# Performance work log

Measured on AMD Instinct MI355X. Metric: run time of the kernel, lower is better.

## Reference

```python
import jax, jax.numpy as jnp
import numpy as np

NUM_HEADS = 16
HIDDEN = 1024
HEAD_DIM = HIDDEN // NUM_HEADS


def setup_inputs() -> dict:
    key = jax.random.key(0)
    ks = jax.random.split(key, 9)
    B, S = 2, 2048
    s = 1.0 / np.sqrt(HIDDEN)
    return {
        "x": jax.random.normal(ks[0], (B, S, HIDDEN), dtype=jnp.float32),
        "Wq": jax.random.normal(ks[1], (HIDDEN, HIDDEN), dtype=jnp.float32) * s,
        "bq": jnp.zeros((HIDDEN,), dtype=jnp.float32),
        "Wk": jax.random.normal(ks[2], (HIDDEN, HIDDEN), dtype=jnp.float32) * s,
        "bk": jnp.zeros((HIDDEN,), dtype=jnp.float32),
        "Wv": jax.random.normal(ks[3], (HIDDEN, HIDDEN), dtype=jnp.float32) * s,
        "bv": jnp.zeros((HIDDEN,), dtype=jnp.float32),
        "Wo": jax.random.normal(ks[4], (HIDDEN, HIDDEN), dtype=jnp.float32) * s,
        "bo": jnp.zeros((HIDDEN,), dtype=jnp.float32),
    }


def reference(x, Wq, bq, Wk, bk, Wv, bv, Wo, bo):
    B, S, H = x.shape
    # project and split heads: [B, S, H] -> [B, nh, S, hd]
    def split_heads(t):
        return t.reshape(B, S, NUM_HEADS, HEAD_DIM).transpose(0, 2, 1, 3)

    q = split_heads(x @ Wq + bq)
    k = split_heads(x @ Wk + bk)
    v = split_heads(x @ Wv + bv)

    scores = jnp.einsum("bhqd,bhkd->bhqk", q, k) / jnp.sqrt(
        jnp.asarray(HEAD_DIM, dtype=x.dtype))
    probs = jax.nn.softmax(scores, axis=-1)
    # attn_drop_rate = 0.0 -> dropout is identity
    ctx = jnp.einsum("bhqk,bhkd->bhqd", probs, v)
    ctx = ctx.transpose(0, 2, 1, 3).reshape(B, S, H)
    out = ctx @ Wo + bo
    return out
```

## Files before the change

kernel.cpp:

```cpp
#include <hip/hip_runtime.h>

#define NHEADS 16
#define HDIM   64
#define SEQL   2048
#define HID    1024
#define NB     2
#define MT     4096

#define QSCALE 0.18033688011112042f
#define RESCALE_THR 6.0f

typedef float        f4_t   __attribute__((ext_vector_type(4)));
typedef unsigned int u32x4  __attribute__((ext_vector_type(4)));
typedef __bf16       bf16x8 __attribute__((ext_vector_type(8)));

typedef const __attribute__((address_space(1))) unsigned int* gas_ptr;
typedef __attribute__((address_space(3))) unsigned int*       las_ptr;

__device__ __forceinline__ void gload16(const void* g, void* l){
  __builtin_amdgcn_global_load_lds((gas_ptr)g, (las_ptr)l, 16, 0, 0);
}
__device__ __forceinline__ unsigned int pkbf(float a, float b){
  unsigned short lo = __builtin_bit_cast(unsigned short, (__bf16)a);
  unsigned short hi = __builtin_bit_cast(unsigned short, (__bf16)b);
  return (unsigned)lo | ((unsigned)hi << 16);
}
__device__ __forceinline__ unsigned short f2bf(float f){
  return __builtin_bit_cast(unsigned short, (__bf16)f);
}
__device__ __forceinline__ u32x4 ld16(const unsigned short* p){
  return *reinterpret_cast<const u32x4*>(p);
}
__device__ __forceinline__ f4_t mfma_bf16(u32x4 a, u32x4 b, f4_t c){
  return __builtin_amdgcn_mfma_f32_16x16x32_bf16(
      __builtin_bit_cast(bf16x8, a), __builtin_bit_cast(bf16x8, b), c, 0, 0, 0);
}

__global__ __launch_bounds__(256) void xcast(const float* __restrict__ x,
                                             unsigned short* __restrict__ xb){
  int gid = blockIdx.x * 256 + threadIdx.x;
  float4 a = reinterpret_cast<const float4*>(x)[gid * 2];
  float4 b = reinterpret_cast<const float4*>(x)[gid * 2 + 1];
  u32x4 o;
  o[0] = pkbf(a.x, a.y);
  o[1] = pkbf(a.z, a.w);
  o[2] = pkbf(b.x, b.y);
  o[3] = pkbf(b.z, b.w);
  *reinterpret_cast<u32x4*>(&xb[gid * 8]) = o;
}

__global__ void prep_w(const float* __restrict__ Wq, const float* __restrict__ Wk,
                       const float* __restrict__ Wv, const float* __restrict__ Wo,
                       unsigned short* __restrict__ wqT, unsigned short* __restrict__ wkT,
                       unsigned short* __restrict__ wvT, unsigned short* __restrict__ woT){
  __shared__ float t[32][33];
  int z = blockIdx.z;
  const float* W = (z==0)?Wq:(z==1)?Wk:(z==2)?Wv:Wo;
  unsigned short* WT = (z==0)?wqT:(z==1)?wkT:(z==2)?wvT:woT;
  float sc = (z==0) ? QSCALE : 1.0f;
  int k0 = blockIdx.x*32, n0 = blockIdx.y*32;
  int tx = threadIdx.x, ty = threadIdx.y;
  #pragma unroll
  for (int ii=0; ii<4; ii++)
    t[ty+ii*8][tx] = W[(k0+ty+ii*8)*HID + n0+tx];
  __syncthreads();
  #pragma unroll
  for (int ii=0; ii<4; ii++)
    WT[(n0+ty+ii*8)*HID + k0+tx] = f2bf(t[tx][ty+ii*8] * sc);
}

__global__ __launch_bounds__(256) void qkv_gemm(
    const unsigned short* __restrict__ xb,
    const unsigned short* __restrict__ wqT, const unsigned short* __restrict__ wkT,
    const unsigned short* __restrict__ wvT,
    const float* __restrict__ bq, const float* __restrict__ bk, const float* __restrict__ bv,
    unsigned short* __restrict__ qo, unsigned short* __restrict__ ko,
    unsigned short* __restrict__ vto){
  __shared__ unsigned short As[128*32];
  __shared__ unsigned short Bs[128*32];
  const int z = blockIdx.z;
  const unsigned short* wT = (z==0)?wqT:(z==1)?wkT:wvT;
  const float* bias = (z==0)?bq:(z==1)?bk:bv;
  const float bscale = (z==0) ? QSCALE : 1.0f;
  const int m0 = blockIdx.x * 128;
  const int n0 = blockIdx.y * 128;
  const int tid = threadIdx.x;
  const int lane = tid & 63, w = tid >> 6;
  const int l15 = lane & 15, lg = lane >> 4;
  const int wr = (w >> 1) * 64, wc = (w & 1) * 64;
  const int srow = w*16 + (lane >> 2);
  const int skc  = (lane & 3) * 8;

  f4_t acc[4][4];
  f4_t z4 = {0.f, 0.f, 0.f, 0.f};
  #pragma unroll
  for (int i=0;i<4;i++)
    #pragma unroll
    for (int j=0;j<4;j++) acc[i][j] = z4;

  for (int kt = 0; kt < HID; kt += 32) {
    __syncthreads();
    #pragma unroll
    for (int c = 0; c < 2; c++) {
      int row = c*64 + srow;
      gload16(&xb[(m0+row)*HID + kt + skc], (char*)As + c*4096 + w*1024);
      gload16(&wT[(n0+row)*HID + kt + skc], (char*)Bs + c*4096 + w*1024);
    }
    __syncthreads();
    u32x4 a[4], b[4];
    #pragma unroll
    for (int i=0;i<4;i++) a[i] = ld16(&As[(wr + i*16 + l15)*32 + lg*8]);
    #pragma unroll
    for (int j=0;j<4;j++) b[j] = ld16(&Bs[(wc + j*16 + l15)*32 + lg*8]);
    #pragma unroll
    for (int i=0;i<4;i++)
      #pragma unroll
      for (int j=0;j<4;j++)
        acc[i][j] = mfma_bf16(a[i], b[j], acc[i][j]);
  }
  if (z == 2) {
    #pragma unroll
    for (int i=0;i<4;i++){
      int mrow = m0 + wr + i*16 + lg*4;
      int b_ = mrow >> 11, s = mrow & 2047;
      #pragma unroll
      for (int j=0;j<4;j++){
        int n = n0 + wc + j*16 + l15;
        float bs = bias[n];
        int h = n >> 6, d = n & 63;
        unsigned int lo = pkbf(acc[i][j][0]+bs, acc[i][j][1]+bs);
        unsigned int hi = pkbf(acc[i][j][2]+bs, acc[i][j][3]+bs);
        unsigned long long v8 = (unsigned long long)lo | ((unsigned long long)hi << 32);
        *reinterpret_cast<unsigned long long*>(
            vto + (((b_*NHEADS + h)*HDIM + d)*SEQL + s)) = v8;
      }
    }
  } else {
    unsigned short* outp = (z==0) ? qo : ko;
    #pragma unroll
    for (int i=0;i<4;i++){
      int mrow = m0 + wr + i*16 + lg*4;
      #pragma unroll
      for (int j=0;j<4;j++){
        int n = n0 + wc + j*16 + l15;
        float bs = bias[n] * bscale;
        int h = n >> 6, d = n & 63;
        #pragma unroll
        for (int r=0;r<4;r++){
          int m = mrow + r;
          int b_ = m >> 11, s = m & 2047;
          outp[(((b_*NHEADS + h)*SEQL) + s)*HDIM + d] = f2bf(acc[i][j][r] + bs);
        }
      }
    }
  }
}

__global__ __launch_bounds__(512) void flash(
    const unsigned short* __restrict__ q,
    const unsigned short* __restrict__ k,
    const unsigned short* __restrict__ vT,
    unsigned short* __restrict__ ctx){
  __shared__ unsigned short Ks[2][4096];
  __shared__ unsigned short Vs[2][4096];
  __shared__ unsigned short Ps[8][1024];
  const int bh = blockIdx.y;
  const int b_ = bh >> 4, h = bh & 15;
  const int tid = threadIdx.x;
  const int w = tid >> 6, lane = tid & 63;
  const int l15 = lane & 15, lg = lane >> 4;
  const int q0 = blockIdx.x*128 + w*16;
  const unsigned short* qb = q + (bh*SEQL + q0)*HDIM;
  const unsigned short* kp = k + bh*SEQL*HDIM;
  const unsigned short* vp = vT + bh*HDIM*SEQL;
  char* pw = (char*)Ps[w];
  const int swz = (l15 & 7) << 4;

  const int sr = w*8 + (lane >> 3);
  const int scol = ((lane & 7) ^ (sr & 7)) * 8;
  const int ldst = w*1024;

  u32x4 qf[2];
  #pragma unroll
  for (int ks=0; ks<2; ks++)
    qf[ks] = ld16(&qb[l15*HDIM + ks*32 + lg*8]);

  float mr = -1e30f, ls = 0.f;
  f4_t oacc[4];
  f4_t z4 = {0.f,0.f,0.f,0.f};
  #pragma unroll
  for (int dt=0;dt<4;dt++) oacc[dt] = z4;

  auto stage = [&](int buf, int kb){
    gload16(kp + (kb + sr)*HDIM + scol, (char*)Ks[buf] + ldst);
    gload16(vp + sr*SEQL + kb + scol,   (char*)Vs[buf] + ldst);
  };

  int cur = 0;
  stage(0, 0);
  __syncthreads();

  for (int kb = 0; kb < SEQL; kb += 64) {
    if (kb + 64 < SEQL) stage(cur^1, kb + 64);
    const char* kbase = (const char*)Ks[cur];
    const char* vbase = (const char*)Vs[cur];

    f4_t sacc[4];
    __builtin_amdgcn_s_setprio(1);
    #pragma unroll
    for (int t=0;t<4;t++){
      u32x4 k0 = *reinterpret_cast<const u32x4*>(kbase + (t*16+l15)*128 + ((lg*16) ^ swz));
      u32x4 k1 = *reinterpret_cast<const u32x4*>(kbase + (t*16+l15)*128 + ((64 + lg*16) ^ swz));
      f4_t s = mfma_bf16(k0, qf[0], z4);
      sacc[t] = mfma_bf16(k1, qf[1], s);
    }
    __builtin_amdgcn_s_setprio(0);

    float vm = sacc[0][0];
    #pragma unroll
    for (int t=0;t<4;t++)
      #pragma unroll
      for (int r=0;r<4;r++) vm = fmaxf(vm, sacc[t][r]);
    vm = fmaxf(vm, __shfl_xor(vm, 16));
    vm = fmaxf(vm, __shfl_xor(vm, 32));
    if (!__all(vm - mr <= RESCALE_THR)) {
      float mnew = fmaxf(mr, vm);
      float scl = exp2f(mr - mnew);
      mr = mnew;
      ls *= scl;
      #pragma unroll
      for (int dt=0;dt<4;dt++) oacc[dt] *= scl;
    }
    float ps = 0.f;
    #pragma unroll
    for (int t=0;t<4;t++)
      #pragma unroll
      for (int r=0;r<4;r++){
        float p = exp2f(sacc[t][r] - mr);
        sacc[t][r] = p;
        ps += p;
      }
    ps += __shfl_xor(ps, 16);
    ps += __shfl_xor(ps, 32);
    ls += ps;
    {
      int rowb = l15*128;
      #pragma unroll
      for (int t=0;t<4;t++){
        unsigned int lo = pkbf(sacc[t][0], sacc[t][1]);
        unsigned int hi = pkbf(sacc[t][2], sacc[t][3]);
        unsigned long long v8 = (unsigned long long)lo | ((unsigned long long)hi << 32);
        *reinterpret_cast<unsigned long long*>(pw + rowb + ((t*32 + lg*8) ^ swz)) = v8;
      }
    }
    u32x4 pf[2];
    #pragma unroll
    for (int ks=0;ks<2;ks++)
      pf[ks] = *reinterpret_cast<const u32x4*>(
          pw + l15*128 + ((ks*64 + lg*16) ^ swz));

    __builtin_amdgcn_s_setprio(1);
    #pragma unroll
    for (int dt=0;dt<4;dt++){
      u32x4 v0 = *reinterpret_cast<const u32x4*>(vbase + (dt*16+l15)*128 + ((lg*16) ^ swz));
      u32x4 v1 = *reinterpret_cast<const u32x4*>(vbase + (dt*16+l15)*128 + ((64 + lg*16) ^ swz));
      f4_t o = mfma_bf16(v0, pf[0], oacc[dt]);
      oacc[dt] = mfma_bf16(v1, pf[1], o);
    }
    __builtin_amdgcn_s_setprio(0);
    __syncthreads();
    cur ^= 1;
  }

  float inv = 1.0f / ls;
  int orow = b_*SEQL + q0 + l15;
  unsigned short* cb = ctx + orow*HID + h*HDIM;
  #pragma unroll
  for (int dt=0;dt<4;dt++){
    unsigned int lo = pkbf(oacc[dt][0]*inv, oacc[dt][1]*inv);
    unsigned int hi = pkbf(oacc[dt][2]*inv, oacc[dt][3]*inv);
    unsigned long long v8 = (unsigned long long)lo | ((unsigned long long)hi << 32);
    *reinterpret_cast<unsigned long long*>(cb + dt*16 + lg*4) = v8;
  }
}

__global__ __launch_bounds__(256) void out_gemm(
    const unsigned short* __restrict__ cb,
    const unsigned short* __restrict__ woT,
    const float* __restrict__ bo,
    float* __restrict__ out){
  __shared__ unsigned short As[128*32];
  __shared__ unsigned short Bs[128*32];
  const int m0 = blockIdx.x * 128;
  const int n0 = blockIdx.y * 128;
  const int tid = threadIdx.x;
  const int lane = tid & 63, w = tid >> 6;
  const int l15 = lane & 15, lg = lane >> 4;
  const int wr = (w >> 1) * 64, wc = (w & 1) * 64;
  const int srow = w*16 + (lane >> 2);
  const int skc  = (lane & 3) * 8;

  f4_t acc[4][4];
  f4_t z4 = {0.f,0.f,0.f,0.f};
  #pragma unroll
  for (int i=0;i<4;i++)
    #pragma unroll
    for (int j=0;j<4;j++) acc[i][j] = z4;

  for (int kt = 0; kt < HID; kt += 32) {
    __syncthreads();
    #pragma unroll
    for (int c = 0; c < 2; c++) {
      int row = c*64 + srow;
      gload16(&cb[(m0+row)*HID + kt + skc],  (char*)As + c*4096 + w*1024);
      gload16(&woT[(n0+row)*HID + kt + skc], (char*)Bs + c*4096 + w*1024);
    }
    __syncthreads();
    u32x4 a[4], b[4];
    #pragma unroll
    for (int i=0;i<4;i++) a[i] = ld16(&As[(wr + i*16 + l15)*32 + lg*8]);
    #pragma unroll
    for (int j=0;j<4;j++) b[j] = ld16(&Bs[(wc + j*16 + l15)*32 + lg*8]);
    #pragma unroll
    for (int i=0;i<4;i++)
      #pragma unroll
      for (int j=0;j<4;j++)
        acc[i][j] = mfma_bf16(a[i], b[j], acc[i][j]);
  }
  #pragma unroll
  for (int i=0;i<4;i++){
    int mrow = m0 + wr + i*16 + lg*4;
    #pragma unroll
    for (int j=0;j<4;j++){
      int n = n0 + wc + j*16 + l15;
      float bs = bo[n];
      #pragma unroll
      for (int r=0;r<4;r++)
        out[(mrow + r)*HID + n] = acc[i][j][r] + bs;
    }
  }
}

extern "C" void kernel_launch(void* const* d_in, const int* in_sizes, int n_in,
                              void* d_out, int out_size, void* d_ws, size_t ws_size,
                              hipStream_t stream){
  const float* x  = (const float*)d_in[0];
  const float* Wq = (const float*)d_in[1];
  const float* bq = (const float*)d_in[2];
  const float* Wk = (const float*)d_in[3];
  const float* bk = (const float*)d_in[4];
  const float* Wv = (const float*)d_in[5];
  const float* bv = (const float*)d_in[6];
  const float* Wo = (const float*)d_in[7];
  const float* bo = (const float*)d_in[8];
  float* out = (float*)d_out;

  char* ws = (char*)d_ws;
  size_t off = 0;
  auto alloc = [&](size_t bytes) -> void* {
    void* p = ws + off;
    off += (bytes + 255) & ~(size_t)255;
    return p;
  };
  unsigned short* xb   = (unsigned short*)alloc((size_t)MT*HID*2);
  unsigned short* wqT  = (unsigned short*)alloc((size_t)HID*HID*2);
  unsigned short* wkT  = (unsigned short*)alloc((size_t)HID*HID*2);
  unsigned short* wvT  = (unsigned short*)alloc((size_t)HID*HID*2);
  unsigned short* woT  = (unsigned short*)alloc((size_t)HID*HID*2);
  unsigned short* q_ws = (unsigned short*)alloc((size_t)MT*HID*2);
  unsigned short* k_ws = (unsigned short*)alloc((size_t)MT*HID*2);
  unsigned short* vT_ws= (unsigned short*)alloc((size_t)MT*HID*2);
  unsigned short* c_ws = (unsigned short*)alloc((size_t)MT*HID*2);

  prep_w<<<dim3(32,32,4), dim3(32,8), 0, stream>>>(Wq,Wk,Wv,Wo, wqT,wkT,wvT,woT);
  xcast<<<dim3(2048), dim3(256), 0, stream>>>(x, xb);
  qkv_gemm<<<dim3(32,8,3), dim3(256), 0, stream>>>(xb, wqT,wkT,wvT, bq,bk,bv,
                                                   q_ws, k_ws, vT_ws);
  flash<<<dim3(16,32), dim3(512), 0, stream>>>(q_ws, k_ws, vT_ws, c_ws);
  out_gemm<<<dim3(32,8), dim3(256), 0, stream>>>(c_ws, woT, bo, out);
}
```

Before: 163.4 us.

## Switch flash attention to 32x32x16 MFMA with register-resident P via permlane swap

Rewrites the flash-attention inner loop to use 32x32x16 bf16 MFMA tiles, with each wave owning 32 query rows instead of 16 and blocks shrunk to 4 waves. The P matrix now stays in registers: accumulator outputs are rearranged into B-operand layout with permlane32 swaps, so the per-wave LDS round trip for probabilities is gone. Row max and sum reductions become mostly in-register, needing only one cross-half shuffle. The cost is more accumulator registers per lane and fewer waves per block, which may reduce latency hiding.

```diff
diff --git a/kernel.cpp b/kernel.cpp
--- a/kernel.cpp
+++ b/kernel.cpp
@@ -11,6 +11,7 @@
 #define RESCALE_THR 6.0f
 
 typedef float        f4_t   __attribute__((ext_vector_type(4)));
+typedef float        f32x16 __attribute__((ext_vector_type(16)));
 typedef unsigned int u32x4  __attribute__((ext_vector_type(4)));
 typedef __bf16       bf16x8 __attribute__((ext_vector_type(8)));
 
@@ -35,6 +36,27 @@
   return __builtin_amdgcn_mfma_f32_16x16x32_bf16(
       __builtin_bit_cast(bf16x8, a), __builtin_bit_cast(bf16x8, b), c, 0, 0, 0);
 }
+__device__ __forceinline__ f32x16 mfma32(u32x4 a, u32x4 b, f32x16 c){
+  return __builtin_amdgcn_mfma_f32_32x32x16_bf16(
+      __builtin_bit_cast(bf16x8, a), __builtin_bit_cast(bf16x8, b), c, 0, 0, 0);
+}
+
+#if __has_builtin(__builtin_amdgcn_permlane32_swap)
+typedef unsigned int u32x2 __attribute__((ext_vector_type(2)));
+__device__ __forceinline__ void plswap(unsigned int &a, unsigned int &b){
+  u32x2 r = __builtin_amdgcn_permlane32_swap(a, b, false, false);
+  a = r[0]; b = r[1];
+}
+#else
+__device__ __forceinline__ void plswap(unsigned int &a, unsigned int &b){
+  unsigned int as = (unsigned int)__shfl_xor((int)a, 32);
+  unsigned int bs = (unsigned int)__shfl_xor((int)b, 32);
+  bool hi = (threadIdx.x & 32) != 0;
+  unsigned int na = hi ? bs : a;
+  unsigned int nb = hi ? b  : as;
+  a = na; b = nb;
+}
+#endif
 
 __global__ __launch_bounds__(256) void xcast(const float* __restrict__ x,
                                              unsigned short* __restrict__ xb){
@@ -156,131 +178,143 @@
   }
 }
 
-__global__ __launch_bounds__(512) void flash(
+__global__ __launch_bounds__(256) void flash(
     const unsigned short* __restrict__ q,
     const unsigned short* __restrict__ k,
     const unsigned short* __restrict__ vT,
     unsigned short* __restrict__ ctx){
   __shared__ unsigned short Ks[2][4096];
   __shared__ unsigned short Vs[2][4096];
-  __shared__ unsigned short Ps[8][1024];
   const int bh = blockIdx.y;
   const int b_ = bh >> 4, h = bh & 15;
   const int tid = threadIdx.x;
   const int w = tid >> 6, lane = tid & 63;
-  const int l15 = lane & 15, lg = lane >> 4;
-  const int q0 = blockIdx.x*128 + w*16;
+  const int l31 = lane & 31, hi = lane >> 5;
+  const int q0 = blockIdx.x*128 + w*32;
   const unsigned short* qb = q + (bh*SEQL + q0)*HDIM;
   const unsigned short* kp = k + bh*SEQL*HDIM;
   const unsigned short* vp = vT + bh*HDIM*SEQL;
-  char* pw = (char*)Ps[w];
-  const int swz = (l15 & 7) << 4;
-
-  const int sr = w*8 + (lane >> 3);
+
+  const int sr = w*16 + (lane >> 3);
   const int scol = ((lane & 7) ^ (sr & 7)) * 8;
-  const int ldst = w*1024;
-
-  u32x4 qf[2];
-  #pragma unroll
-  for (int ks=0; ks<2; ks++)
-    qf[ks] = ld16(&qb[l15*HDIM + ks*32 + lg*8]);
-
-  float mr = -1e30f, ls = 0.f;
-  f4_t oacc[4];
-  f4_t z4 = {0.f,0.f,0.f,0.f};
-  #pragma unroll
-  for (int dt=0;dt<4;dt++) oacc[dt] = z4;
+  const int ldst = w*2048;
+
+  u32x4 qf[4];
+  #pragma unroll
+  for (int c=0;c<4;c++)
+    qf[c] = ld16(&qb[l31*HDIM + c*16 + hi*8]);
+
+  float mr = -1e30f, lsum = 0.f;
+  f32x16 oacc[2];
+  f32x16 z16 = {0.f,0.f,0.f,0.f,0.f,0.f,0.f,0.f,0.f,0.f,0.f,0.f,0.f,0.f,0.f,0.f};
+  oacc[0] = z16; oacc[1] = z16;
 
   auto stage = [&](int buf, int kb){
-    gload16(kp + (kb + sr)*HDIM + scol, (char*)Ks[buf] + ldst);
-    gload16(vp + sr*SEQL + kb + scol,   (char*)Vs[buf] + ldst);
+    const unsigned short* gk = kp + (kb + sr)*HDIM + scol;
+    gload16(gk,          (char*)Ks[buf] + ldst);
+    gload16(gk + 8*HDIM, (char*)Ks[buf] + ldst + 1024);
+    const unsigned short* gv = vp + sr*SEQL + kb + scol;
+    gload16(gv,          (char*)Vs[buf] + ldst);
+    gload16(gv + 8*SEQL, (char*)Vs[buf] + ldst + 1024);
   };
 
   int cur = 0;
   stage(0, 0);
   __syncthreads();
+
+  const int rs = (l31 & 7) << 4;
 
   for (int kb = 0; kb < SEQL; kb += 64) {
     if (kb + 64 < SEQL) stage(cur^1, kb + 64);
     const char* kbase = (const char*)Ks[cur];
     const char* vbase = (const char*)Vs[cur];
 
-    f4_t sacc[4];
+    f32x16 sacc[2];
     __builtin_amdgcn_s_setprio(1);
     #pragma unroll
-    for (int t=0;t<4;t++){
-      u32x4 k0 = *reinterpret_cast<const u32x4*>(kbase + (t*16+l15)*128 + ((lg*16) ^ swz));
-      u32x4 k1 = *reinterpret_cast<const u32x4*>(kbase + (t*16+l15)*128 + ((64 + lg*16) ^ swz));
-      f4_t s = mfma_bf16(k0, qf[0], z4);
-      sacc[t] = mfma_bf16(k1, qf[1], s);
+    for (int t=0;t<2;t++){
+      const char* rowb = kbase + (t*32 + l31)*128;
+      #pragma unroll
+      for (int c=0;c<4;c++){
+        u32x4 kf = *reinterpret_cast<const u32x4*>(rowb + ((c*32 + hi*16) ^ rs));
+        sacc[t] = (c==0) ? mfma32(kf, qf[0], z16) : mfma32(kf, qf[c], sacc[t]);
+      }
     }
     __builtin_amdgcn_s_setprio(0);
 
-    float vm = sacc[0][0];
-    #pragma unroll
-    for (int t=0;t<4;t++)
-      #pragma unroll
-      for (int r=0;r<4;r++) vm = fmaxf(vm, sacc[t][r]);
-    vm = fmaxf(vm, __shfl_xor(vm, 16));
+    float mx[16];
+    #pragma unroll
+    for (int r=0;r<16;r++) mx[r] = fmaxf(sacc[0][r], sacc[1][r]);
+    #pragma unroll
+    for (int r=0;r<8;r++) mx[r] = fmaxf(mx[r], mx[r+8]);
+    #pragma unroll
+    for (int r=0;r<4;r++) mx[r] = fmaxf(mx[r], mx[r+4]);
+    float vm = fmaxf(fmaxf(mx[0], mx[1]), fmaxf(mx[2], mx[3]));
     vm = fmaxf(vm, __shfl_xor(vm, 32));
     if (!__all(vm - mr <= RESCALE_THR)) {
       float mnew = fmaxf(mr, vm);
       float scl = exp2f(mr - mnew);
       mr = mnew;
-      ls *= scl;
-      #pragma unroll
-      for (int dt=0;dt<4;dt++) oacc[dt] *= scl;
-    }
-    float ps = 0.f;
-    #pragma unroll
-    for (int t=0;t<4;t++)
-      #pragma unroll
-      for (int r=0;r<4;r++){
-        float p = exp2f(sacc[t][r] - mr);
-        sacc[t][r] = p;
-        ps += p;
+      lsum *= scl;
+      oacc[0] *= scl;
+      oacc[1] *= scl;
+    }
+    float sm[16];
+    #pragma unroll
+    for (int t=0;t<2;t++)
+      #pragma unroll
+      for (int r=0;r<16;r++) sacc[t][r] = exp2f(sacc[t][r] - mr);
+    #pragma unroll
+    for (int r=0;r<16;r++) sm[r] = sacc[0][r] + sacc[1][r];
+    #pragma unroll
+    for (int r=0;r<8;r++) sm[r] += sm[r+8];
+    #pragma unroll
+    for (int r=0;r<4;r++) sm[r] += sm[r+4];
+    float ps = (sm[0] + sm[1]) + (sm[2] + sm[3]);
+    ps += __shfl_xor(ps, 32);
+    lsum += ps;
+
+    u32x4 pa[4];
+    #pragma unroll
+    for (int t=0;t<2;t++)
+      #pragma unroll
+      for (int hf=0;hf<2;hf++){
+        unsigned int c1 = pkbf(sacc[t][hf*8+0], sacc[t][hf*8+1]);
+        unsigned int c2 = pkbf(sacc[t][hf*8+2], sacc[t][hf*8+3]);
+        unsigned int c3 = pkbf(sacc[t][hf*8+4], sacc[t][hf*8+5]);
+        unsigned int c4 = pkbf(sacc[t][hf*8+6], sacc[t][hf*8+7]);
+        plswap(c1, c3);
+        plswap(c2, c4);
+        u32x4 f; f[0]=c1; f[1]=c2; f[2]=c3; f[3]=c4;
+        pa[t*2+hf] = f;
       }
-    ps += __shfl_xor(ps, 16);
-    ps += __shfl_xor(ps, 32);
-    ls += ps;
-    {
-      int rowb = l15*128;
-      #pragma unroll
-      for (int t=0;t<4;t++){
-        unsigned int lo = pkbf(sacc[t][0], sacc[t][1]);
-        unsigned int hi = pkbf(sacc[t][2], sacc[t][3]);
-        unsigned long long v8 = (unsigned long long)lo | ((unsigned long long)hi << 32);
-        *reinterpret_cast<unsigned long long*>(pw + rowb + ((t*32 + lg*8) ^ swz)) = v8;
+
+    __builtin_amdgcn_s_setprio(1);
+    #pragma unroll
+    for (int dt=0;dt<2;dt++){
+      const char* rowb = vbase + (dt*32 + l31)*128;
+      #pragma unroll
+      for (int ks=0;ks<4;ks++){
+        u32x4 vf = *reinterpret_cast<const u32x4*>(rowb + ((ks*32 + hi*16) ^ rs));
+        oacc[dt] = mfma32(vf, pa[ks], oacc[dt]);
       }
-    }
-    u32x4 pf[2];
-    #pragma unroll
-    for (int ks=0;ks<2;ks++)
-      pf[ks] = *reinterpret_cast<const u32x4*>(
-          pw + l15*128 + ((ks*64 + lg*16) ^ swz));
-
-    __builtin_amdgcn_s_setprio(1);
-    #pragma unroll
-    for (int dt=0;dt<4;dt++){
-      u32x4 v0 = *reinterpret_cast<const u32x4*>(vbase + (dt*16+l15)*128 + ((lg*16) ^ swz));
-      u32x4 v1 = *reinterpret_cast<const u32x4*>(vbase + (dt*16+l15)*128 + ((64 + lg*16) ^ swz));
-      f4_t o = mfma_bf16(v0, pf[0], oacc[dt]);
-      oacc[dt] = mfma_bf16(v1, pf[1], o);
     }
     __builtin_amdgcn_s_setprio(0);
     __syncthreads();
     cur ^= 1;
   }
 
-  float inv = 1.0f / ls;
-  int orow = b_*SEQL + q0 + l15;
-  unsigned short* cb = ctx + orow*HID + h*HDIM;
-  #pragma unroll
-  for (int dt=0;dt<4;dt++){
-    unsigned int lo = pkbf(oacc[dt][0]*inv, oacc[dt][1]*inv);
-    unsigned int hi = pkbf(oacc[dt][2]*inv, oacc[dt][3]*inv);
-    unsigned long long v8 = (unsigned long long)lo | ((unsigned long long)hi << 32);
-    *reinterpret_cast<unsigned long long*>(cb + dt*16 + lg*4) = v8;
+  float inv = 1.0f / lsum;
+  unsigned short* cb = ctx + (b_*SEQL + q0 + l31)*HID + h*HDIM;
+  #pragma unroll
+  for (int dt=0;dt<2;dt++){
+    #pragma unroll
+    for (int kq=0;kq<4;kq++){
+      unsigned int lo = pkbf(oacc[dt][kq*4+0]*inv, oacc[dt][kq*4+1]*inv);
+      unsigned int hi2 = pkbf(oacc[dt][kq*4+2]*inv, oacc[dt][kq*4+3]*inv);
+      unsigned long long v8 = (unsigned long long)lo | ((unsigned long long)hi2 << 32);
+      *reinterpret_cast<unsigned long long*>(cb + dt*32 + kq*8 + hi*4) = v8;
+    }
   }
 }
 
@@ -376,6 +410,6 @@
   xcast<<<dim3(2048), dim3(256), 0, stream>>>(x, xb);
   qkv_gemm<<<dim3(32,8,3), dim3(256), 0, stream>>>(xb, wqT,wkT,wvT, bq,bk,bv,
                                                    q_ws, k_ws, vT_ws);
-  flash<<<dim3(16,32), dim3(512), 0, stream>>>(q_ws, k_ws, vT_ws, c_ws);
+  flash<<<dim3(16,32), dim3(256), 0, stream>>>(q_ws, k_ws, vT_ws, c_ws);
   out_gemm<<<dim3(32,8), dim3(256), 0, stream>>>(c_ws, woT, bo, out);
 }
```

Result: slower. 170.2 us (+4.2%).
